# Kernel tuning notes

Measured on AMD Instinct MI355X. Metric: run time of the kernel, lower is better.

The kernel has to match this reference:

```python
import jax, jax.numpy as jnp
import numpy as np

EMBED_DIM = 1024
NUM_HEADS = 16
HEAD_DIM = EMBED_DIM // NUM_HEADS
HIDDEN_DIM = 4096


def layer_norm(x, gamma, beta, eps=1e-5):
    mu = jnp.mean(x, axis=-1, keepdims=True)
    var = jnp.var(x, axis=-1, keepdims=True)
    return (x - mu) * jax.lax.rsqrt(var + eps) * gamma + beta


def setup_inputs() -> dict:
    key = jax.random.key(0)
    ks = jax.random.split(key, 12)
    D, H3, F = EMBED_DIM, 3 * EMBED_DIM, HIDDEN_DIM
    s_d = 1.0 / np.sqrt(D)
    s_f = 1.0 / np.sqrt(F)
    return {
        "x": jax.random.normal(ks[0], (2, 2048, D), dtype=jnp.float32),
        "w_qkv": jax.random.uniform(ks[1], (D, H3), jnp.float32, -s_d, s_d),
        "b_qkv": jax.random.uniform(ks[2], (H3,), jnp.float32, -s_d, s_d),
        "w_out": jax.random.uniform(ks[3], (D, D), jnp.float32, -s_d, s_d),
        "b_out": jax.random.uniform(ks[4], (D,), jnp.float32, -s_d, s_d),
        "w_fc1": jax.random.uniform(ks[5], (D, F), jnp.float32, -s_d, s_d),
        "b_fc1": jax.random.uniform(ks[6], (F,), jnp.float32, -s_d, s_d),
        "w_fc2": jax.random.uniform(ks[7], (F, D), jnp.float32, -s_f, s_f),
        "b_fc2": jax.random.uniform(ks[8], (D,), jnp.float32, -s_f, s_f),
        "ln1_g": jnp.ones((D,), jnp.float32),
        "ln1_b": jnp.zeros((D,), jnp.float32),
        "ln2_g": jnp.ones((D,), jnp.float32),
        "ln2_b": jnp.zeros((D,), jnp.float32),
    }


def reference(x, w_qkv, b_qkv, w_out, b_out, w_fc1, b_fc1, w_fc2, b_fc2,
              ln1_g, ln1_b, ln2_g, ln2_b):
    B, N, D = x.shape
    H, Hd = NUM_HEADS, HEAD_DIM

    # --- attention branch (pre-LN) ---
    h = layer_norm(x, ln1_g, ln1_b)
    qkv = h @ w_qkv + b_qkv                              # [B,N,3D]
    qkv = qkv.reshape(B, N, 3, H, Hd).transpose(2, 0, 3, 1, 4)  # [3,B,H,N,Hd]
    q, k, v = qkv[0], qkv[1], qkv[2]
    scores = jnp.einsum("bhnd,bhmd->bhnm", q, k) * (Hd ** -0.5)  # [B,H,N,N]
    attn = jax.nn.softmax(scores, axis=-1)
    out = jnp.einsum("bhnm,bhmd->bhnd", attn, v)         # [B,H,N,Hd]
    out = out.transpose(0, 2, 1, 3).reshape(B, N, D)
    x = x + (out @ w_out + b_out)

    # --- FFN branch (pre-LN) ---
    h = layer_norm(x, ln2_g, ln2_b)
    h = jax.nn.gelu(h @ w_fc1 + b_fc1, approximate=False)  # torch F.gelu default (erf)
    x = x + (h @ w_fc2 + b_fc2)
    return x
```

## Files before the change

kernel.cpp:

```cpp
#include <hip/hip_runtime.h>
#include <hip/hip_bf16.h>

#define D_ 1024
#define F_ 4096
#define NH 16
#define HD 64
#define SEQ 2048
#define TOK 4096

typedef short bf16x8 __attribute__((ext_vector_type(8)));
typedef float f32x4 __attribute__((ext_vector_type(4)));
typedef unsigned int u32x4 __attribute__((ext_vector_type(4)));

static __device__ __forceinline__ f32x4 mfma16(bf16x8 a, bf16x8 b, f32x4 c) {
  return __builtin_amdgcn_mfma_f32_16x16x32_bf16(a, b, c, 0, 0, 0);
}

static __device__ __forceinline__ unsigned short f2bf(float f) {
  union { float f; unsigned int u; } a; a.f = f;
  unsigned int u = a.u;
  u += 0x7fffu + ((u >> 16) & 1u);
  return (unsigned short)(u >> 16);
}

static __device__ __forceinline__ unsigned int cvtpk(float lo, float hi) {
  unsigned int r;
  asm("v_cvt_pk_bf16_f32 %0, %1, %2" : "=v"(r) : "v"(lo), "v"(hi));
  return r;
}

#define AS1 __attribute__((address_space(1)))
#define AS3 __attribute__((address_space(3)))
static __device__ __forceinline__ void gld16(const void* g, void* l) {
  __builtin_amdgcn_global_load_lds((const AS1 unsigned int*)(uintptr_t)(g),
                                   (AS3 unsigned int*)(uintptr_t)(l), 16, 0, 0);
}

#define WAITBAR_CNT()                                    \
  do {                                                   \
    asm volatile("s_waitcnt vmcnt(4)" ::: "memory");     \
    __builtin_amdgcn_s_barrier();                        \
    __builtin_amdgcn_sched_barrier(0);                   \
  } while (0)
#define WAITBAR0()                                       \
  do {                                                   \
    asm volatile("s_waitcnt vmcnt(0)" ::: "memory");     \
    __builtin_amdgcn_s_barrier();                        \
    __builtin_amdgcn_sched_barrier(0);                   \
  } while (0)

__global__ void transpose_all(const float* __restrict__ wqkv, const float* __restrict__ wout,
                              const float* __restrict__ wfc1, const float* __restrict__ wfc2,
                              unsigned short* __restrict__ oqkv, unsigned short* __restrict__ oout,
                              unsigned short* __restrict__ ofc1, unsigned short* __restrict__ ofc2) {
  __shared__ float tile[32][33];
  int idx = blockIdx.x;
  const float* in;
  unsigned short* out;
  int K, N;
  if (idx < 3072)      { in = wqkv; out = oqkv; K = 1024; N = 3072; }
  else if (idx < 4096) { in = wout; out = oout; K = 1024; N = 1024; idx -= 3072; }
  else if (idx < 8192) { in = wfc1; out = ofc1; K = 1024; N = 4096; idx -= 4096; }
  else                 { in = wfc2; out = ofc2; K = 4096; N = 1024; idx -= 8192; }
  int nt = N >> 5;
  int n0 = (idx % nt) * 32, k0 = (idx / nt) * 32;
  int tx = threadIdx.x, ty = threadIdx.y;
#pragma unroll
  for (int i = 0; i < 32; i += 8)
    tile[ty + i][tx] = in[(size_t)(k0 + ty + i) * N + n0 + tx];
  __syncthreads();
#pragma unroll
  for (int i = 0; i < 32; i += 8)
    out[(size_t)(n0 + ty + i) * K + k0 + tx] = f2bf(tile[tx][ty + i]);
}

__global__ __launch_bounds__(256) void layernorm_bf16(const float* __restrict__ x,
                                                      const float* __restrict__ g,
                                                      const float* __restrict__ bta,
                                                      unsigned short* __restrict__ out) {
  int wv = threadIdx.x >> 6, lane = threadIdx.x & 63;
  int row = blockIdx.x * 4 + wv;
  const float4* xr = (const float4*)(x + (size_t)row * D_);
  float4 v[4];
  float s = 0.f, ss = 0.f;
#pragma unroll
  for (int i = 0; i < 4; i++) {
    v[i] = xr[i * 64 + lane];
    s += v[i].x + v[i].y + v[i].z + v[i].w;
    ss += v[i].x * v[i].x + v[i].y * v[i].y + v[i].z * v[i].z + v[i].w * v[i].w;
  }
#pragma unroll
  for (int off = 32; off >= 1; off >>= 1) {
    s += __shfl_xor(s, off);
    ss += __shfl_xor(ss, off);
  }
  float mu = s * (1.0f / D_);
  float var = ss * (1.0f / D_) - mu * mu;
  float r = rsqrtf(var + 1e-5f);
#pragma unroll
  for (int i = 0; i < 4; i++) {
    int col = i * 256 + lane * 4;
    unsigned short ob[4];
    ob[0] = f2bf((v[i].x - mu) * r * g[col + 0] + bta[col + 0]);
    ob[1] = f2bf((v[i].y - mu) * r * g[col + 1] + bta[col + 1]);
    ob[2] = f2bf((v[i].z - mu) * r * g[col + 2] + bta[col + 2]);
    ob[3] = f2bf((v[i].w - mu) * r * g[col + 3] + bta[col + 3]);
    *(ushort4*)(out + (size_t)row * D_ + col) = *(ushort4*)ob;
  }
}

__global__ __launch_bounds__(256) void ln2_fused(const float* __restrict__ xin,
                                                 const float* __restrict__ p,
                                                 const float* __restrict__ g,
                                                 const float* __restrict__ bta,
                                                 float* __restrict__ x1out,
                                                 unsigned short* __restrict__ out) {
  int wv = threadIdx.x >> 6, lane = threadIdx.x & 63;
  int row = blockIdx.x * 4 + wv;
  const float4* xr = (const float4*)(xin + (size_t)row * D_);
  const float4* pr = (const float4*)(p + (size_t)row * D_);
  float4* xw = (float4*)(x1out + (size_t)row * D_);
  float4 v[4];
  float s = 0.f, ss = 0.f;
#pragma unroll
  for (int i = 0; i < 4; i++) {
    float4 a = xr[i * 64 + lane], b = pr[i * 64 + lane];
    v[i] = make_float4(a.x + b.x, a.y + b.y, a.z + b.z, a.w + b.w);
    xw[i * 64 + lane] = v[i];
    s += v[i].x + v[i].y + v[i].z + v[i].w;
    ss += v[i].x * v[i].x + v[i].y * v[i].y + v[i].z * v[i].z + v[i].w * v[i].w;
  }
#pragma unroll
  for (int off = 32; off >= 1; off >>= 1) {
    s += __shfl_xor(s, off);
    ss += __shfl_xor(ss, off);
  }
  float mu = s * (1.0f / D_);
  float var = ss * (1.0f / D_) - mu * mu;
  float r = rsqrtf(var + 1e-5f);
#pragma unroll
  for (int i = 0; i < 4; i++) {
    int col = i * 256 + lane * 4;
    unsigned short ob[4];
    ob[0] = f2bf((v[i].x - mu) * r * g[col + 0] + bta[col + 0]);
    ob[1] = f2bf((v[i].y - mu) * r * g[col + 1] + bta[col + 1]);
    ob[2] = f2bf((v[i].z - mu) * r * g[col + 2] + bta[col + 2]);
    ob[3] = f2bf((v[i].w - mu) * r * g[col + 3] + bta[col + 3]);
    *(ushort4*)(out + (size_t)row * D_ + col) = *(ushort4*)ob;
  }
}

__global__ __launch_bounds__(256) void reduce_add(float4* __restrict__ out,
                                                  const float4* __restrict__ p1) {
#pragma unroll
  for (int j = 0; j < 4; ++j) {
    int i = blockIdx.x * 1024 + j * 256 + threadIdx.x;
    float4 o = out[i], a = p1[i];
    out[i] = make_float4(o.x + a.x, o.y + a.y, o.z + a.z, o.w + a.w);
  }
}

template <int MODE, int NBUF>
__global__ __launch_bounds__(256, (NBUF == 2 ? 4 : 3)) void gemm_bt(
    const unsigned short* __restrict__ A, const unsigned short* __restrict__ Bt,
    const float* __restrict__ bias, const float* __restrict__ resid,
    void* __restrict__ outp, float* __restrict__ p1, int M, int N, int K, int KSPL) {
  __shared__ __align__(16) char a_lds[NBUF * 8192];
  __shared__ __align__(16) char b_lds[NBUF * 8192];
  const int t = threadIdx.x;
  const int lane = t & 63, w = t >> 6;
  const int g = lane >> 4, lr = lane & 15;
  const int wm = (w >> 1) * 64, wn = (w & 1) * 64;
  const int n0 = blockIdx.x * 128, m0 = blockIdx.y * 128;
  const int z = blockIdx.z;
  const int kt0 = z * KSPL, nIter = KSPL / 32;

  const int mac0 = t >> 3;
  const int v0 = ((t & 7) ^ (mac0 & 7)) << 4;
  const int grow0 = mac0 + ((v0 >> 6) << 6);
  const int cc0 = v0 & 63;
  const char* srcA0 = (const char*)A + ((size_t)(m0 + grow0) * K + kt0) * 2 + cc0;
  const char* srcA1 = srcA0 + (size_t)32 * K * 2;
  const char* srcB0 = (const char*)Bt + ((size_t)(n0 + grow0) * K + kt0) * 2 + cc0;
  const char* srcB1 = srcB0 + (size_t)32 * K * 2;

  const int rdA = lr * 128 + (((wm & 64) + g * 16) ^ ((lr & 7) << 4));
  const int rdB = lr * 128 + (((wn & 64) + g * 16) ^ ((lr & 7) << 4));

#define STAGE(IT, BO)                                                    \
  do {                                                                   \
    size_t kb = (size_t)(IT) * 64;                                       \
    gld16(srcA0 + kb, a_lds + (BO) + t * 16);                            \
    gld16(srcA1 + kb, a_lds + (BO) + 4096 + t * 16);                     \
    gld16(srcB0 + kb, b_lds + (BO) + t * 16);                            \
    gld16(srcB1 + kb, b_lds + (BO) + 4096 + t * 16);                     \
  } while (0)

#define GSTEP(BO)                                                          \
  do {                                                                     \
    bf16x8 af[4], bfr[4];                                                  \
    _Pragma("unroll") for (int mi = 0; mi < 4; mi++)                       \
        af[mi] = *(const bf16x8*)(a_lds + (BO) + rdA + mi * 2048);         \
    _Pragma("unroll") for (int ni = 0; ni < 4; ni++)                       \
        bfr[ni] = *(const bf16x8*)(b_lds + (BO) + rdB + ni * 2048);        \
    _Pragma("unroll") for (int mi = 0; mi < 4; mi++)                       \
        _Pragma("unroll") for (int ni = 0; ni < 4; ni++)                   \
            acc[mi][ni] = mfma16(af[mi], bfr[ni], acc[mi][ni]);            \
  } while (0)

  f32x4 acc[4][4] = {};
  if constexpr (NBUF == 2) {
    STAGE(0, 0);
    int cur = 0;
#pragma unroll 1
    for (int it = 0; it < nIter; ++it) {
      WAITBAR0();
      if (it + 1 < nIter) STAGE(it + 1, (cur ^ 1) * 8192);
      GSTEP(cur * 8192);
      cur ^= 1;
    }
  } else {
    STAGE(0, 0);
    STAGE(1, 8192);
    int bo0 = 0, bo1 = 8192, bo2 = 16384;
#pragma unroll 1
    for (int it = 0; it < nIter - 1; ++it) {
      WAITBAR_CNT();
      if (it + 2 < nIter) STAGE(it + 2, bo2);
      GSTEP(bo0);
      int tmp = bo0; bo0 = bo1; bo1 = bo2; bo2 = tmp;
    }
    WAITBAR0();
    GSTEP(bo0);
  }
#undef STAGE
#undef GSTEP

#pragma unroll
  for (int mi = 0; mi < 4; mi++) {
#pragma unroll
    for (int ni = 0; ni < 4; ni++) {
#pragma unroll
      for (int j = 0; j < 4; j++) {
        int row = m0 + wm + mi * 16 + g * 4 + j;
        int col = n0 + wn + ni * 16 + lr;
        float val = acc[mi][ni][j];
        if (MODE == 0) {
          val += bias[col];
          int which = col >> 10, cc = col & 1023;
          int hh = cc >> 6, dd = cc & 63;
          int bb = row >> 11, nn = row & 2047;
          size_t base = (size_t)which * (TOK * D_);
          if (which == 2) {
            int off = nn & 63;
            int cpos = (off & 35) | ((off & 4) << 1) | ((off & 8) << 1) | ((off & 16) >> 2);
            ((unsigned short*)outp)[base + ((size_t)(bb * NH + hh) * HD + dd) * SEQ +
                                    (nn & ~63) + cpos] = f2bf(val);
          } else {
            if (which == 0) val *= 0.18033688011112042f;
            ((unsigned short*)outp)[base + (((size_t)(bb * NH + hh) * SEQ + nn) << 6) + dd] =
                f2bf(val);
          }
        } else if (MODE == 2) {
          val += bias[col];
          val = 0.5f * val * (1.0f + erff(val * 0.70710678118f));
          ((unsigned short*)outp)[(size_t)row * N + col] = f2bf(val);
        } else if (MODE == 5 || MODE == 6) {
          if (z == 0) {
            val += bias[col] + resid[(size_t)row * N + col];
            ((float*)outp)[(size_t)row * N + col] = val;
          } else {
            p1[(size_t)row * N + col] = val;
          }
        }
      }
    }
  }
}

__global__ __launch_bounds__(256, 4) void attn_kernel(const unsigned short* __restrict__ q,
                                                      const unsigned short* __restrict__ k,
                                                      const unsigned short* __restrict__ vT,
                                                      unsigned short* __restrict__ ao) {
  __shared__ __align__(16) char ldsb[32768];
  const int t = threadIdx.x, lane = t & 63, w = t >> 6;
  const int g = lane >> 4, lr = lane & 15;
  const int bid = (blockIdx.x & 7) * 128 + (blockIdx.x >> 3);
  const int qt = bid & 31, bh = bid >> 5;
  const int bb = bh >> 4, hh = bh & 15;

  const unsigned short* qp = q + ((size_t)bh * SEQ + qt * 64 + w * 16) * HD;
  bf16x8 qf0 = *(const bf16x8*)(qp + lr * HD + g * 8);
  bf16x8 qf1 = *(const bf16x8*)(qp + lr * HD + 32 + g * 8);

  f32x4 oacc[4] = {};
  f32x4 spv = {0.f, 0.f, 0.f, 0.f};

  const int srow = t >> 3, sc = (t & 7) << 4;
  const int ssw = sc ^ ((srow & 7) << 4);
  const char* kgl = (const char*)(k + (size_t)bh * SEQ * HD) + srow * 128 + ssw;
  const char* vgl = (const char*)(vT + (size_t)bh * HD * SEQ) + (size_t)srow * 4096 + ssw;
  char* kdst = ldsb + w * 1024;
  char* vdst = ldsb + 16384 + w * 1024;

  const int rsw = (lr & 7) << 4;
  const char* r0 = ldsb + lr * 128 + ((g * 16) ^ rsw);
  const char* r1 = ldsb + lr * 128 + ((64 + g * 16) ^ rsw);

#define ISSUE(BUF)                                   \
  do {                                               \
    gld16(kgl, kdst + (BUF) * 8192);                 \
    gld16(kgl + 4096, kdst + (BUF) * 8192 + 4096);   \
    gld16(vgl, vdst + (BUF) * 8192);                 \
    gld16(vgl + 131072, vdst + (BUF) * 8192 + 4096); \
    kgl += 8192;                                     \
    vgl += 128;                                      \
  } while (0)

#define COMPUTE(BUF)                                                                     \
  do {                                                                                   \
    f32x4 sT[4];                                                                         \
    __builtin_amdgcn_s_setprio(1);                                                       \
    _Pragma("unroll") for (int sb = 0; sb < 4; ++sb) {                                   \
      bf16x8 kf0 = *(const bf16x8*)(r0 + (BUF) * 8192 + sb * 2048);                      \
      bf16x8 kf1 = *(const bf16x8*)(r1 + (BUF) * 8192 + sb * 2048);                      \
      f32x4 zz = {};                                                                     \
      zz = mfma16(kf0, qf0, zz);                                                         \
      sT[sb] = mfma16(kf1, qf1, zz);                                                     \
    }                                                                                    \
    __builtin_amdgcn_s_setprio(0);                                                       \
    float p[4][4];                                                                       \
    _Pragma("unroll") for (int sb = 0; sb < 4; ++sb) _Pragma("unroll")                   \
        for (int jr = 0; jr < 4; ++jr) {                                                 \
      p[sb][jr] = exp2f(sT[sb][jr]);                                                     \
      spv[jr] += p[sb][jr];                                                              \
    }                                                                                    \
    u32x4 pA[2];                                                                         \
    _Pragma("unroll") for (int kk = 0; kk < 2; ++kk) pA[kk] =                            \
        (u32x4){cvtpk(p[2 * kk][0], p[2 * kk][1]), cvtpk(p[2 * kk][2], p[2 * kk][3]),    \
                cvtpk(p[2 * kk + 1][0], p[2 * kk + 1][1]),                               \
                cvtpk(p[2 * kk + 1][2], p[2 * kk + 1][3])};                              \
    __builtin_amdgcn_s_setprio(1);                                                       \
    _Pragma("unroll") for (int vb = 0; vb < 4; ++vb) {                                   \
      bf16x8 v0 = *(const bf16x8*)(r0 + 16384 + (BUF) * 8192 + vb * 2048);               \
      bf16x8 v1 = *(const bf16x8*)(r1 + 16384 + (BUF) * 8192 + vb * 2048);               \
      oacc[vb] = mfma16(__builtin_bit_cast(bf16x8, pA[0]), v0, oacc[vb]);                \
      oacc[vb] = mfma16(__builtin_bit_cast(bf16x8, pA[1]), v1, oacc[vb]);                \
    }                                                                                    \
    __builtin_amdgcn_s_setprio(0);                                                       \
  } while (0)

  ISSUE(0);

  int staged = 1;
#pragma unroll 1
  for (int i2 = 0; i2 < SEQ / 128; ++i2) {
    WAITBAR0();
    if (staged < SEQ / 64) { ISSUE(1); ++staged; }
    COMPUTE(0);
    WAITBAR0();
    if (staged < SEQ / 64) { ISSUE(0); ++staged; }
    COMPUTE(1);
  }
#undef ISSUE
#undef COMPUTE

  float sp = (spv[0] + spv[1]) + (spv[2] + spv[3]);
  sp += __shfl_xor(sp, 16);
  sp += __shfl_xor(sp, 32);

#pragma unroll
  for (int jj = 0; jj < 4; ++jj) {
    float li = 1.0f / __shfl(sp, g * 4 + jj);
    int nrow = qt * 64 + w * 16 + g * 4 + jj;
#pragma unroll
    for (int vb = 0; vb < 4; ++vb)
      ao[((size_t)bb * SEQ + nrow) * D_ + hh * HD + vb * 16 + lr] = f2bf(oacc[vb][jj] * li);
  }
}

extern "C" void kernel_launch(void* const* d_in, const int* in_sizes, int n_in,
                              void* d_out, int out_size, void* d_ws, size_t ws_size,
                              hipStream_t stream) {
  const float* x     = (const float*)d_in[0];
  const float* w_qkv = (const float*)d_in[1];
  const float* b_qkv = (const float*)d_in[2];
  const float* w_out = (const float*)d_in[3];
  const float* b_out = (const float*)d_in[4];
  const float* w_fc1 = (const float*)d_in[5];
  const float* b_fc1 = (const float*)d_in[6];
  const float* w_fc2 = (const float*)d_in[7];
  const float* b_fc2 = (const float*)d_in[8];
  const float* ln1_g = (const float*)d_in[9];
  const float* ln1_b = (const float*)d_in[10];
  const float* ln2_g = (const float*)d_in[11];
  const float* ln2_b = (const float*)d_in[12];
  float* out = (float*)d_out;

  char* ws = (char*)d_ws;
  unsigned short* wqkvT = (unsigned short*)(ws);
  unsigned short* woutT = (unsigned short*)(ws + 6291456);
  unsigned short* wfc1T = (unsigned short*)(ws + 8388608);
  unsigned short* wfc2T = (unsigned short*)(ws + 16777216);
  unsigned short* h     = (unsigned short*)(ws + 25165824);
  unsigned short* qkv   = (unsigned short*)(ws + 33554432);
  unsigned short* ao    = (unsigned short*)(ws + 58720256);
  float*          x1    = (float*)(ws + 67108864);
  unsigned short* hg    = (unsigned short*)(ws + 83886080);
  float* p_op  = (float*)(ws + 83886080);
  float* p_fc1 = (float*)(ws);

  transpose_all<<<12288, dim3(32, 8), 0, stream>>>(w_qkv, w_out, w_fc1, w_fc2,
                                                   wqkvT, woutT, wfc1T, wfc2T);

  layernorm_bf16<<<TOK / 4, 256, 0, stream>>>(x, ln1_g, ln1_b, h);
  gemm_bt<0, 3><<<dim3(24, 32, 1), 256, 0, stream>>>(h, wqkvT, b_qkv, nullptr, qkv, nullptr,
                                                     TOK, 3072, 1024, 1024);
  attn_kernel<<<1024, 256, 0, stream>>>(qkv, qkv + (size_t)TOK * D_, qkv + 2 * (size_t)TOK * D_,
                                        ao);
  gemm_bt<5, 3><<<dim3(8, 32, 2), 256, 0, stream>>>(ao, woutT, b_out, x, x1, p_op,
                                                    TOK, 1024, 1024, 512);
  ln2_fused<<<TOK / 4, 256, 0, stream>>>(x1, p_op, ln2_g, ln2_b, x1, h);
  gemm_bt<2, 2><<<dim3(32, 32, 1), 256, 0, stream>>>(h, wfc1T, b_fc1, nullptr, hg, nullptr,
                                                     TOK, 4096, 1024, 1024);
  gemm_bt<6, 3><<<dim3(8, 32, 2), 256, 0, stream>>>(hg, wfc2T, b_fc2, x1, out, p_fc1,
                                                    TOK, 1024, 4096, 2048);
  reduce_add<<<1024, 256, 0, stream>>>((float4*)out, (const float4*)p_fc1);
}
```

Before: 266.7 us.

## Give each attention wave two query blocks to reuse K/V LDS fragments

The attention kernel now runs with 2 waves per block instead of 4, and each wave handles 32 query rows (two 16-row blocks) instead of 16. Each K and V fragment read from LDS feeds MFMAs for both query blocks, which halves LDS reads per unit of work. Because there are half as many waves, each thread now issues twice as many global-to-LDS loads per stage. The cost is higher register pressure, with doubled accumulators and Q fragments, and fewer resident waves per CU to hide latency, since each block still uses the same 32KB of LDS.

```diff
diff --git a/kernel.cpp b/kernel.cpp
--- a/kernel.cpp
+++ b/kernel.cpp
@@ -278,7 +278,7 @@
   }
 }
 
-__global__ __launch_bounds__(256, 4) void attn_kernel(const unsigned short* __restrict__ q,
+__global__ __launch_bounds__(128, 2) void attn_kernel(const unsigned short* __restrict__ q,
                                                       const unsigned short* __restrict__ k,
                                                       const unsigned short* __restrict__ vT,
                                                       unsigned short* __restrict__ ao) {
@@ -289,15 +289,19 @@
   const int qt = bid & 31, bh = bid >> 5;
   const int bb = bh >> 4, hh = bh & 15;
 
-  const unsigned short* qp = q + ((size_t)bh * SEQ + qt * 64 + w * 16) * HD;
-  bf16x8 qf0 = *(const bf16x8*)(qp + lr * HD + g * 8);
-  bf16x8 qf1 = *(const bf16x8*)(qp + lr * HD + 32 + g * 8);
-
-  f32x4 oacc[4] = {};
-  f32x4 spv = {0.f, 0.f, 0.f, 0.f};
-
-  const int srow = t >> 3, sc = (t & 7) << 4;
-  const int ssw = sc ^ ((srow & 7) << 4);
+  const unsigned short* qp = q + ((size_t)bh * SEQ + qt * 64 + w * 32) * HD;
+  bf16x8 qf[2][2];
+#pragma unroll
+  for (int qb = 0; qb < 2; ++qb)
+#pragma unroll
+    for (int hf = 0; hf < 2; ++hf)
+      qf[qb][hf] = *(const bf16x8*)(qp + (qb * 16 + lr) * HD + hf * 32 + g * 8);
+
+  f32x4 oacc[2][4] = {};
+  f32x4 spv[2] = {};
+
+  const int srow = t >> 3;
+  const int ssw = ((t & 7) << 4) ^ ((srow & 7) << 4);
   const char* kgl = (const char*)(k + (size_t)bh * SEQ * HD) + srow * 128 + ssw;
   const char* vgl = (const char*)(vT + (size_t)bh * HD * SEQ) + (size_t)srow * 4096 + ssw;
   char* kdst = ldsb + w * 1024;
@@ -307,47 +311,52 @@
   const char* r0 = ldsb + lr * 128 + ((g * 16) ^ rsw);
   const char* r1 = ldsb + lr * 128 + ((64 + g * 16) ^ rsw);
 
-#define ISSUE(BUF)                                   \
-  do {                                               \
-    gld16(kgl, kdst + (BUF) * 8192);                 \
-    gld16(kgl + 4096, kdst + (BUF) * 8192 + 4096);   \
-    gld16(vgl, vdst + (BUF) * 8192);                 \
-    gld16(vgl + 131072, vdst + (BUF) * 8192 + 4096); \
-    kgl += 8192;                                     \
-    vgl += 128;                                      \
+#define ISSUE(BUF)                                                      \
+  do {                                                                  \
+    _Pragma("unroll") for (int r = 0; r < 4; ++r) {                     \
+      gld16(kgl + r * 2048, kdst + (BUF) * 8192 + r * 2048);            \
+      gld16(vgl + r * 65536, vdst + (BUF) * 8192 + r * 2048);           \
+    }                                                                   \
+    kgl += 8192;                                                        \
+    vgl += 128;                                                         \
   } while (0)
 
 #define COMPUTE(BUF)                                                                     \
   do {                                                                                   \
-    f32x4 sT[4];                                                                         \
+    f32x4 sT[2][4];                                                                      \
     __builtin_amdgcn_s_setprio(1);                                                       \
     _Pragma("unroll") for (int sb = 0; sb < 4; ++sb) {                                   \
       bf16x8 kf0 = *(const bf16x8*)(r0 + (BUF) * 8192 + sb * 2048);                      \
       bf16x8 kf1 = *(const bf16x8*)(r1 + (BUF) * 8192 + sb * 2048);                      \
-      f32x4 zz = {};                                                                     \
-      zz = mfma16(kf0, qf0, zz);                                                         \
-      sT[sb] = mfma16(kf1, qf1, zz);                                                     \
+      f32x4 z0 = {};                                                                     \
+      z0 = mfma16(kf0, qf[0][0], z0);                                                    \
+      sT[0][sb] = mfma16(kf1, qf[0][1], z0);                                             \
+      f32x4 z1 = {};                                                                     \
+      z1 = mfma16(kf0, qf[1][0], z1);                                                    \
+      sT[1][sb] = mfma16(kf1, qf[1][1], z1);                                             \
     }                                                                                    \
     __builtin_amdgcn_s_setprio(0);                                                       \
-    float p[4][4];                                                                       \
-    _Pragma("unroll") for (int sb = 0; sb < 4; ++sb) _Pragma("unroll")                   \
-        for (int jr = 0; jr < 4; ++jr) {                                                 \
-      p[sb][jr] = exp2f(sT[sb][jr]);                                                     \
-      spv[jr] += p[sb][jr];                                                              \
+    _Pragma("unroll") for (int qb = 0; qb < 2; ++qb) {                                   \
+      float p[4][4];                                                                     \
+      _Pragma("unroll") for (int sb = 0; sb < 4; ++sb) _Pragma("unroll")                 \
+          for (int jr = 0; jr < 4; ++jr) {                                               \
+        p[sb][jr] = exp2f(sT[qb][sb][jr]);                                               \
+        spv[qb][jr] += p[sb][jr];                                                        \
+      }                                                                                  \
+      u32x4 pA[2];                                                                       \
+      _Pragma("unroll") for (int kk = 0; kk < 2; ++kk) pA[kk] =                          \
+          (u32x4){cvtpk(p[2 * kk][0], p[2 * kk][1]), cvtpk(p[2 * kk][2], p[2 * kk][3]),  \
+                  cvtpk(p[2 * kk + 1][0], p[2 * kk + 1][1]),                             \
+                  cvtpk(p[2 * kk + 1][2], p[2 * kk + 1][3])};                            \
+      __builtin_amdgcn_s_setprio(1);                                                     \
+      _Pragma("unroll") for (int vb = 0; vb < 4; ++vb) {                                 \
+        bf16x8 v0 = *(const bf16x8*)(r0 + 16384 + (BUF) * 8192 + vb * 2048);             \
+        bf16x8 v1 = *(const bf16x8*)(r1 + 16384 + (BUF) * 8192 + vb * 2048);             \
+        oacc[qb][vb] = mfma16(__builtin_bit_cast(bf16x8, pA[0]), v0, oacc[qb][vb]);      \
+        oacc[qb][vb] = mfma16(__builtin_bit_cast(bf16x8, pA[1]), v1, oacc[qb][vb]);      \
+      }                                                                                  \
+      __builtin_amdgcn_s_setprio(0);                                                     \
     }                                                                                    \
-    u32x4 pA[2];                                                                         \
-    _Pragma("unroll") for (int kk = 0; kk < 2; ++kk) pA[kk] =                            \
-        (u32x4){cvtpk(p[2 * kk][0], p[2 * kk][1]), cvtpk(p[2 * kk][2], p[2 * kk][3]),    \
-                cvtpk(p[2 * kk + 1][0], p[2 * kk + 1][1]),                               \
-                cvtpk(p[2 * kk + 1][2], p[2 * kk + 1][3])};                              \
-    __builtin_amdgcn_s_setprio(1);                                                       \
-    _Pragma("unroll") for (int vb = 0; vb < 4; ++vb) {                                   \
-      bf16x8 v0 = *(const bf16x8*)(r0 + 16384 + (BUF) * 8192 + vb * 2048);               \
-      bf16x8 v1 = *(const bf16x8*)(r1 + 16384 + (BUF) * 8192 + vb * 2048);               \
-      oacc[vb] = mfma16(__builtin_bit_cast(bf16x8, pA[0]), v0, oacc[vb]);                \
-      oacc[vb] = mfma16(__builtin_bit_cast(bf16x8, pA[1]), v1, oacc[vb]);                \
-    }                                                                                    \
-    __builtin_amdgcn_s_setprio(0);                                                       \
   } while (0)
 
   ISSUE(0);
@@ -365,17 +374,20 @@
 #undef ISSUE
 #undef COMPUTE
 
-  float sp = (spv[0] + spv[1]) + (spv[2] + spv[3]);
-  sp += __shfl_xor(sp, 16);
-  sp += __shfl_xor(sp, 32);
-
-#pragma unroll
-  for (int jj = 0; jj < 4; ++jj) {
-    float li = 1.0f / __shfl(sp, g * 4 + jj);
-    int nrow = qt * 64 + w * 16 + g * 4 + jj;
-#pragma unroll
-    for (int vb = 0; vb < 4; ++vb)
-      ao[((size_t)bb * SEQ + nrow) * D_ + hh * HD + vb * 16 + lr] = f2bf(oacc[vb][jj] * li);
+#pragma unroll
+  for (int qb = 0; qb < 2; ++qb) {
+    float sp = (spv[qb][0] + spv[qb][1]) + (spv[qb][2] + spv[qb][3]);
+    sp += __shfl_xor(sp, 16);
+    sp += __shfl_xor(sp, 32);
+#pragma unroll
+    for (int jj = 0; jj < 4; ++jj) {
+      float li = 1.0f / __shfl(sp, g * 4 + jj);
+      int nrow = qt * 64 + w * 32 + qb * 16 + g * 4 + jj;
+#pragma unroll
+      for (int vb = 0; vb < 4; ++vb)
+        ao[((size_t)bb * SEQ + nrow) * D_ + hh * HD + vb * 16 + lr] =
+            f2bf(oacc[qb][vb][jj] * li);
+    }
   }
 }
 
@@ -416,7 +428,7 @@
   layernorm_bf16<<<TOK / 4, 256, 0, stream>>>(x, ln1_g, ln1_b, h);
   gemm_bt<0, 3><<<dim3(24, 32, 1), 256, 0, stream>>>(h, wqkvT, b_qkv, nullptr, qkv, nullptr,
                                                      TOK, 3072, 1024, 1024);
-  attn_kernel<<<1024, 256, 0, stream>>>(qkv, qkv + (size_t)TOK * D_, qkv + 2 * (size_t)TOK * D_,
+  attn_kernel<<<1024, 128, 0, stream>>>(qkv, qkv + (size_t)TOK * D_, qkv + 2 * (size_t)TOK * D_,
                                         ao);
   gemm_bt<5, 3><<<dim3(8, 32, 2), 256, 0, stream>>>(ao, woutT, b_out, x, x1, p_op,
                                                     TOK, 1024, 1024, 512);
```

New measurement: 277.8 us. 4.1% more time.
